# Kernel optimization log

Hardware: AMD Instinct MI355X
Metric: run time of the kernel (lower is better)

## Reference

```python
import jax, jax.numpy as jnp
import numpy as np

# dims
B_, L_, DIN, H, DOUT, NL = 2, 1024, 512, 768, 512, 4
ED, N, K = H, 16, 4            # expand_factor=1 -> d_inner=H; d_state=16; d_conv=4
DTR = (H + 15) // 16           # dt_rank = ceil(d_model/16) = 48


def setup_inputs() -> dict:
    key = jax.random.key(0)
    ks = iter(jax.random.split(key, 32))
    def g(shape, s=0.02):
        return jax.random.normal(next(ks), shape, jnp.float32) * s
    inp = dict(
        x=jax.random.normal(next(ks), (B_, L_, DIN), jnp.float32),
        in_proj_w=g((H, DIN)), in_proj_b=jnp.zeros((H,), jnp.float32),
        out_proj_w=g((DOUT, H)), out_proj_b=jnp.zeros((DOUT,), jnp.float32),
        ln1_w=jnp.ones((NL, H), jnp.float32), ln1_b=jnp.zeros((NL, H), jnp.float32),
        ln2_w=jnp.ones((NL, H), jnp.float32), ln2_b=jnp.zeros((NL, H), jnp.float32),
        ffn_w1=g((NL, 4 * H, H)), ffn_b1=jnp.zeros((NL, 4 * H), jnp.float32),
        ffn_w2=g((NL, H, 4 * H)), ffn_b2=jnp.zeros((NL, H), jnp.float32),
        rms_w=jnp.ones((NL, ED), jnp.float32),
        m_in_w=g((NL, 2 * ED, H)),
        conv_w=g((NL, ED, 1, K), 0.2), conv_b=jnp.zeros((NL, ED), jnp.float32),
        xproj_w=g((NL, DTR + 2 * N, ED)),
        dt_w=g((NL, ED, DTR), 0.1), dt_b=g((NL, ED), 0.1),
        A_log=jnp.log(jnp.tile(jnp.arange(1, N + 1, dtype=jnp.float32), (NL, ED, 1))),
        Dp=jnp.ones((NL, ED), jnp.float32),
        m_out_w=g((NL, H, ED)),
    )
    return inp


def _layernorm(x, w, b):
    m = x.mean(-1, keepdims=True)
    v = ((x - m) ** 2).mean(-1, keepdims=True)
    return (x - m) / jnp.sqrt(v + 1e-5) * w + b


def _rmsnorm(x, w):
    return x * jax.lax.rsqrt((x * x).mean(-1, keepdims=True) + 1e-5) * w


def _selective_scan(dA, dBx):
    # h_t = dA_t * h_{t-1} + dBx_t, done as a parallel associative scan over L
    def comb(c1, c2):
        a1, b1 = c1
        a2, b2 = c2
        return a1 * a2, a2 * b1 + b2
    _, h = jax.lax.associative_scan(comb, (dA, dBx), axis=1)
    return h  # (B, L, ED, N)


def _mamba(x, rw, iw, cw, cb, xw, dw, db, Alog, Dp, ow):
    # mambapy ResidualBlock: x + MambaBlock(RMSNorm(x))
    xn = _rmsnorm(x, rw)
    xz = xn @ iw.T                             # (B, L, 2*ED)
    xi, z = jnp.split(xz, 2, axis=-1)
    # causal depthwise conv1d (padding = K-1 left)
    xc = jax.lax.conv_general_dilated(
        xi.transpose(0, 2, 1), cw, (1,), [(K - 1, 0)],
        feature_group_count=ED, dimension_numbers=('NCH', 'OIH', 'NCH'))
    xi = jax.nn.silu(xc.transpose(0, 2, 1) + cb)
    dbc = xi @ xw.T                            # (B, L, DTR + 2N)
    d = dbc[..., :DTR]
    Bm = dbc[..., DTR:DTR + N]
    Cm = dbc[..., DTR + N:]
    delta = jax.nn.softplus(d @ dw.T + db)     # (B, L, ED)
    A = -jnp.exp(Alog)                         # (ED, N)
    dA = jnp.exp(delta[..., None] * A)         # (B, L, ED, N)
    dBx = (delta * xi)[..., None] * Bm[:, :, None, :]
    h = _selective_scan(dA, dBx)
    y = jnp.einsum('blen,bln->ble', h, Cm) + Dp * xi
    y = y * jax.nn.silu(z)
    return x + y @ ow.T


def reference(x, in_proj_w, in_proj_b, out_proj_w, out_proj_b,
              ln1_w, ln1_b, ln2_w, ln2_b,
              ffn_w1, ffn_b1, ffn_w2, ffn_b2,
              rms_w, m_in_w, conv_w, conv_b, xproj_w,
              dt_w, dt_b, A_log, Dp, m_out_w):
    h = x @ in_proj_w.T + in_proj_b
    for i in range(NL):
        h = h + _mamba(_layernorm(h, ln1_w[i], ln1_b[i]),
                       rms_w[i], m_in_w[i], conv_w[i], conv_b[i], xproj_w[i],
                       dt_w[i], dt_b[i], A_log[i], Dp[i], m_out_w[i])
        hn = _layernorm(h, ln2_w[i], ln2_b[i])
        h = h + jax.nn.relu(hn @ ffn_w1[i].T + ffn_b1[i]) @ ffn_w2[i].T + ffn_b2[i]
    return h @ out_proj_w.T + out_proj_b
```

## Files before the change

kernel.cpp:

```cpp
#include <hip/hip_runtime.h>
#include <stdint.h>

typedef unsigned short u16;
typedef __attribute__((ext_vector_type(8))) short short8;
typedef __attribute__((ext_vector_type(4))) float f32x4;

static __device__ __forceinline__ u16 f2bf(float f){
  unsigned int x = __float_as_uint(f);
  unsigned int r = (x + 0x7FFFu + ((x >> 16) & 1u)) >> 16;
  return (u16)r;
}
static __device__ __forceinline__ float bf2f(u16 u){
  return __uint_as_float(((unsigned int)u) << 16);
}

__global__ __launch_bounds__(256) void prep_cvt(
    const float* __restrict__ s0, const float* __restrict__ s1,
    const float* __restrict__ s2, const float* __restrict__ s3,
    const float* __restrict__ s4, const float* __restrict__ s5,
    const float* __restrict__ s6,
    u16* __restrict__ d0, u16* __restrict__ d1, u16* __restrict__ d2,
    u16* __restrict__ d3, u16* __restrict__ d4, u16* __restrict__ d5,
    u16* __restrict__ d6){
  size_t i = ((size_t)blockIdx.x * 256 + threadIdx.x) * 8;
  const float* src; u16* dst; size_t base;
  if      (i <  1048576){ src = s0; dst = d0; base = 0; }
  else if (i <  1441792){ src = s1; dst = d1; base = 1048576; }
  else if (i <  1835008){ src = s2; dst = d2; base = 1441792; }
  else if (i <  6553600){ src = s3; dst = d3; base = 1835008; }
  else if (i <  8912896){ src = s4; dst = d4; base = 6553600; }
  else if (i < 18350080){ src = s5; dst = d5; base = 8912896; }
  else                  { src = s6; dst = d6; base = 18350080; }
  size_t o = i - base;
  #pragma unroll
  for (int p = 0; p < 2; p++){
    float4 v = *reinterpret_cast<const float4*>(src + o + p * 4);
    union { u16 u[4]; unsigned long long ll; } t;
    t.u[0] = f2bf(v.x); t.u[1] = f2bf(v.y); t.u[2] = f2bf(v.z); t.u[3] = f2bf(v.w);
    *reinterpret_cast<unsigned long long*>(dst + o + p * 4) = t.ll;
  }
}

__global__ __launch_bounds__(256) void build_dbc(const float* __restrict__ dt_w,
                                                 const float* __restrict__ xproj_w,
                                                 u16* __restrict__ out){
  const int total = 4 * 896 * 768;
  for (int idx = blockIdx.x * 256 + threadIdx.x; idx < total; idx += gridDim.x * 256){
    int l = idx / (896 * 768);
    int rem = idx - l * 896 * 768;
    int row = rem / 768;
    int k = rem - row * 768;
    float v = 0.f;
    if (row < 768){
      const float* dtr = dt_w + ((size_t)l * 768 + row) * 48;
      const float* xp  = xproj_w + (size_t)l * 80 * 768 + k;
      #pragma unroll 8
      for (int j = 0; j < 48; j++) v += dtr[j] * xp[(size_t)j * 768];
    } else if (row < 800){
      v = xproj_w[(size_t)l * 80 * 768 + (size_t)(48 + row - 768) * 768 + k];
    }
    out[idx] = f2bf(v);
  }
}

__global__ __launch_bounds__(256) void ln_rms_kernel(const float* __restrict__ in,
                                                     const float* __restrict__ w,
                                                     const float* __restrict__ b,
                                                     const float* __restrict__ rw,
                                                     float* __restrict__ xln,
                                                     u16* __restrict__ outB){
  int row = blockIdx.x;
  const float* x = in + (size_t)row * 768;
  int t = threadIdx.x;
  float v0 = x[t], v1 = x[t + 256], v2 = x[t + 512];
  float s = v0 + v1 + v2;
  float s2 = v0 * v0 + v1 * v1 + v2 * v2;
  #pragma unroll
  for (int off = 1; off < 64; off <<= 1){ s += __shfl_xor(s, off); s2 += __shfl_xor(s2, off); }
  __shared__ float red[8];
  int wid = t >> 6, lane = t & 63;
  if (lane == 0){ red[wid] = s; red[4 + wid] = s2; }
  __syncthreads();
  s = red[0] + red[1] + red[2] + red[3];
  s2 = red[4] + red[5] + red[6] + red[7];
  float mean = s * (1.f / 768.f);
  float var = s2 * (1.f / 768.f) - mean * mean;
  float rstd = rsqrtf(var + 1e-5f);
  float o0 = (v0 - mean) * rstd * w[t] + b[t];
  float o1 = (v1 - mean) * rstd * w[t + 256] + b[t + 256];
  float o2 = (v2 - mean) * rstd * w[t + 512] + b[t + 512];
  xln[(size_t)row * 768 + t]       = o0;
  xln[(size_t)row * 768 + t + 256] = o1;
  xln[(size_t)row * 768 + t + 512] = o2;
  float q = o0 * o0 + o1 * o1 + o2 * o2;
  #pragma unroll
  for (int off = 1; off < 64; off <<= 1){ q += __shfl_xor(q, off); }
  __syncthreads();
  if (lane == 0) red[wid] = q;
  __syncthreads();
  q = red[0] + red[1] + red[2] + red[3];
  float rs = rsqrtf(q * (1.f / 768.f) + 1e-5f);
  outB[(size_t)row * 768 + t]       = f2bf(o0 * rs * rw[t]);
  outB[(size_t)row * 768 + t + 256] = f2bf(o1 * rs * rw[t + 256]);
  outB[(size_t)row * 768 + t + 512] = f2bf(o2 * rs * rw[t + 512]);
}

__global__ __launch_bounds__(256) void ln_kernel(const float* __restrict__ in,
                                                 const float* __restrict__ w,
                                                 const float* __restrict__ b,
                                                 u16* __restrict__ outB){
  int row = blockIdx.x;
  const float* x = in + (size_t)row * 768;
  int t = threadIdx.x;
  float v0 = x[t], v1 = x[t + 256], v2 = x[t + 512];
  float s = v0 + v1 + v2;
  float s2 = v0 * v0 + v1 * v1 + v2 * v2;
  #pragma unroll
  for (int off = 1; off < 64; off <<= 1){ s += __shfl_xor(s, off); s2 += __shfl_xor(s2, off); }
  __shared__ float red[8];
  int wid = t >> 6, lane = t & 63;
  if (lane == 0){ red[wid] = s; red[4 + wid] = s2; }
  __syncthreads();
  s = red[0] + red[1] + red[2] + red[3];
  s2 = red[4] + red[5] + red[6] + red[7];
  float mean = s * (1.f / 768.f);
  float var = s2 * (1.f / 768.f) - mean * mean;
  float rstd = rsqrtf(var + 1e-5f);
  #pragma unroll
  for (int j = 0; j < 3; j++){
    int e = t + j * 256;
    float v = (j == 0) ? v0 : (j == 1) ? v1 : v2;
    outB[(size_t)row * 768 + e] = f2bf((v - mean) * rstd * w[e] + b[e]);
  }
}

__global__ __launch_bounds__(256) void conv_silu(const u16* __restrict__ xzb,
                                                 const float* __restrict__ cw,
                                                 const float* __restrict__ cb,
                                                 u16* __restrict__ xi,
                                                 u16* __restrict__ zs){
  int row = blockIdx.x;
  int b = row >> 10, l = row & 1023;
  for (int e = threadIdx.x; e < 768; e += 256){
    const float* w = cw + (size_t)e * 4;
    float acc = cb[e];
    #pragma unroll
    for (int k = 0; k < 4; k++){
      int ls = l - 3 + k;
      if (ls >= 0) acc += w[k] * bf2f(xzb[((size_t)((b << 10) + ls)) * 1536 + e]);
    }
    float sv = acc / (1.f + __expf(-acc));
    xi[(size_t)row * 768 + e] = f2bf(sv);
    float z = bf2f(xzb[(size_t)row * 1536 + 768 + e]);
    zs[(size_t)row * 768 + e] = f2bf(z / (1.f + __expf(-z)));
  }
}

__global__ __launch_bounds__(256) void scan_pass1(const float* __restrict__ delta,
                                                  const u16* __restrict__ xi,
                                                  const float* __restrict__ bc,
                                                  const float* __restrict__ A_log,
                                                  float2* __restrict__ ab){
  int bid = blockIdx.x;
  int eg = bid % 3; int c = (bid / 3) & 31; int b = bid / 96;
  int e = eg * 256 + threadIdx.x;
  float A[16], a[16], s[16];
  const float* al = A_log + (size_t)e * 16;
  #pragma unroll
  for (int n = 0; n < 16; n++){ A[n] = -__expf(al[n]); a[n] = 1.f; s[n] = 0.f; }
  for (int ll = 0; ll < 32; ll++){
    int row = b * 1024 + c * 32 + ll;
    float dlt = delta[(size_t)row * 768 + e];
    float xiv = bf2f(xi[(size_t)row * 768 + e]);
    float du = dlt * xiv;
    const float* bm = bc + (size_t)row * 32;
    #pragma unroll
    for (int n = 0; n < 16; n++){
      float dA = __expf(dlt * A[n]);
      s[n] = dA * s[n] + du * bm[n];
      a[n] *= dA;
    }
  }
  size_t base = (((size_t)(b * 32 + c) * 768) + e) * 16;
  #pragma unroll
  for (int n = 0; n < 16; n++){ ab[base + n] = make_float2(a[n], s[n]); }
}

__global__ __launch_bounds__(128) void scan_pass2(const float2* __restrict__ ab,
                                                  float* __restrict__ h0){
  int idx = blockIdx.x * 128 + threadIdx.x;
  int b = idx / 12288;
  int en = idx - b * 12288;
  float h = 0.f;
  for (int c = 0; c < 32; c++){
    size_t i = ((size_t)(b * 32 + c) * 12288) + en;
    h0[i] = h;
    float2 v = ab[i];
    h = v.x * h + v.y;
  }
}

__global__ __launch_bounds__(256) void scan_pass3(const float* __restrict__ delta,
                                                  const u16* __restrict__ xi,
                                                  const float* __restrict__ bc,
                                                  const float* __restrict__ A_log,
                                                  const float* __restrict__ h0,
                                                  const float* __restrict__ Dp,
                                                  const u16* __restrict__ zs,
                                                  u16* __restrict__ y){
  int bid = blockIdx.x;
  int eg = bid % 3; int c = (bid / 3) & 31; int b = bid / 96;
  int e = eg * 256 + threadIdx.x;
  float A[16], s[16];
  const float* al = A_log + (size_t)e * 16;
  #pragma unroll
  for (int n = 0; n < 16; n++) A[n] = -__expf(al[n]);
  size_t base = (((size_t)(b * 32 + c) * 768) + e) * 16;
  #pragma unroll
  for (int n = 0; n < 16; n++) s[n] = h0[base + n];
  float dp = Dp[e];
  for (int ll = 0; ll < 32; ll++){
    int row = b * 1024 + c * 32 + ll;
    float dlt = delta[(size_t)row * 768 + e];
    float xiv = bf2f(xi[(size_t)row * 768 + e]);
    float du = dlt * xiv;
    const float* bm = bc + (size_t)row * 32;
    const float* cm = bm + 16;
    float acc = 0.f;
    #pragma unroll
    for (int n = 0; n < 16; n++){
      float dA = __expf(dlt * A[n]);
      s[n] = dA * s[n] + du * bm[n];
      acc += s[n] * cm[n];
    }
    float yv = acc + dp * xiv;
    yv *= bf2f(zs[(size_t)row * 768 + e]);
    y[(size_t)row * 768 + e] = f2bf(yv);
  }
}

template<int MODE, int TS>
__global__ __launch_bounds__(256, 2) void gemmT(
    const u16* __restrict__ A, const u16* __restrict__ Bw, int N, int Kd,
    float* __restrict__ outF, u16* __restrict__ outB,
    const float* __restrict__ bias, const float* __restrict__ r1,
    const float* __restrict__ r2,
    float* __restrict__ dl, float* __restrict__ bco, const float* __restrict__ dtb){
  constexpr int NBUF = (TS == 64) ? 4 : 3;
  constexpr int DEPTH = NBUF - 1;
  constexpr int MI = TS / 32;
  __shared__ u16 sm[NBUF][2 * TS * 64];
  const int tid = threadIdx.x;
  const int wid = tid >> 6, lane = tid & 63;
  const int lhi = lane >> 4, llo = lane & 15;
  const int wm = (wid >> 1) * (TS / 2), wn = (wid & 1) * (TS / 2);
  int nwg = (int)(gridDim.x * gridDim.y);
  int orig = (int)(blockIdx.y * gridDim.x + blockIdx.x);
  int wg = (orig & 7) * (nwg >> 3) + (orig >> 3);
  int gx = (int)gridDim.x;
  int bx = wg % gx, by = wg / gx;
  const int m0 = bx * TS, n0 = by * TS;
  const int nk = Kd >> 6;
  f32x4 acc[MI][MI] = {};

  auto stage = [&](int buf, int kt){
    const u16* Ab = A + (size_t)m0 * Kd + kt * 64;
    const u16* Bb = Bw + (size_t)n0 * Kd + kt * 64;
    u16* basep = &sm[buf][0];
    #pragma unroll
    for (int j = 0; j < TS / 32; j++){
      int sl = j * 256 + tid;
      int row = sl >> 3;
      int ch = (sl & 7) ^ (row & 7);
      __builtin_amdgcn_global_load_lds(
          (const __attribute__((address_space(1))) void*)(Ab + (size_t)row * Kd + ch * 8),
          (__attribute__((address_space(3))) void*)(basep + sl * 8), 16, 0, 0);
    }
    #pragma unroll
    for (int j = 0; j < TS / 32; j++){
      int sl = j * 256 + tid;
      int row = sl >> 3;
      int ch = (sl & 7) ^ (row & 7);
      __builtin_amdgcn_global_load_lds(
          (const __attribute__((address_space(1))) void*)(Bb + (size_t)row * Kd + ch * 8),
          (__attribute__((address_space(3))) void*)(basep + TS * 64 + sl * 8), 16, 0, 0);
    }
  };

  #pragma unroll
  for (int t = 0; t < DEPTH; t++) stage(t, t);
  for (int kt = 0; kt < nk; ++kt){
    if constexpr (TS == 64){
      if (kt + 2 < nk)      asm volatile("s_waitcnt vmcnt(8)" ::: "memory");
      else if (kt + 1 < nk) asm volatile("s_waitcnt vmcnt(4)" ::: "memory");
      else                  asm volatile("s_waitcnt vmcnt(0)" ::: "memory");
    } else {
      if (kt + 1 < nk)      asm volatile("s_waitcnt vmcnt(8)" ::: "memory");
      else                  asm volatile("s_waitcnt vmcnt(0)" ::: "memory");
    }
    __builtin_amdgcn_s_barrier();
    __builtin_amdgcn_sched_barrier(0);
    if (kt + DEPTH < nk) stage((kt + DEPTH) % NBUF, kt + DEPTH);
    const u16* Asb = &sm[kt % NBUF][0];
    const u16* Bsb = &sm[kt % NBUF][TS * 64];
    short8 af[MI][2], bfr[MI][2];
    #pragma unroll
    for (int mi = 0; mi < MI; mi++){
      int row = wm + mi * 16 + llo;
      const u16* rp = Asb + row * 64;
      #pragma unroll
      for (int s2 = 0; s2 < 2; s2++){
        int ch = (s2 * 4 + lhi) ^ (row & 7);
        af[mi][s2] = *(const short8*)(rp + ch * 8);
      }
    }
    #pragma unroll
    for (int ni = 0; ni < MI; ni++){
      int row = wn + ni * 16 + llo;
      const u16* rp = Bsb + row * 64;
      #pragma unroll
      for (int s2 = 0; s2 < 2; s2++){
        int ch = (s2 * 4 + lhi) ^ (row & 7);
        bfr[ni][s2] = *(const short8*)(rp + ch * 8);
      }
    }
    #pragma unroll
    for (int s2 = 0; s2 < 2; s2++)
      #pragma unroll
      for (int mi = 0; mi < MI; mi++)
        #pragma unroll
        for (int ni = 0; ni < MI; ni++)
          acc[mi][ni] = __builtin_amdgcn_mfma_f32_16x16x32_bf16(
              af[mi][s2], bfr[ni][s2], acc[mi][ni], 0, 0, 0);
  }
  #pragma unroll
  for (int mi = 0; mi < MI; mi++){
    #pragma unroll
    for (int ni = 0; ni < MI; ni++){
      int r0 = m0 + wm + mi * 16 + lhi * 4;
      int c = n0 + wn + ni * 16 + llo;
      #pragma unroll
      for (int r = 0; r < 4; r++){
        int rr = r0 + r;
        float v = acc[mi][ni][r];
        if (MODE == 0){
          size_t idx = (size_t)rr * N + c;
          if (bias) v += bias[c];
          if (r1) v += r1[idx];
          if (r2) v += r2[idx];
          outF[idx] = v;
          if (outB) outB[idx] = f2bf(v);
        } else if (MODE == 1){
          size_t idx = (size_t)rr * N + c;
          v += bias[c];
          outB[idx] = f2bf(v > 0.f ? v : 0.f);
        } else if (MODE == 3){
          outB[(size_t)rr * N + c] = f2bf(v);
        } else {
          if (c < 768){
            float tv = v + dtb[c];
            dl[(size_t)rr * 768 + c] = (tv > 20.f) ? tv : log1pf(__expf(tv));
          } else if (c < 800){
            bco[(size_t)rr * 32 + (c - 768)] = v;
          }
        }
      }
    }
  }
}

extern "C" void kernel_launch(void* const* d_in, const int* in_sizes, int n_in,
                              void* d_out, int out_size, void* d_ws, size_t ws_size,
                              hipStream_t stream){
  (void)in_sizes; (void)n_in; (void)out_size; (void)ws_size;
  const float* x_f       = (const float*)d_in[0];
  const float* in_proj_w = (const float*)d_in[1];
  const float* in_proj_b = (const float*)d_in[2];
  const float* out_proj_w= (const float*)d_in[3];
  const float* out_proj_b= (const float*)d_in[4];
  const float* ln1_w     = (const float*)d_in[5];
  const float* ln1_b     = (const float*)d_in[6];
  const float* ln2_w     = (const float*)d_in[7];
  const float* ln2_b     = (const float*)d_in[8];
  const float* ffn_w1    = (const float*)d_in[9];
  const float* ffn_b1    = (const float*)d_in[10];
  const float* ffn_w2    = (const float*)d_in[11];
  const float* ffn_b2    = (const float*)d_in[12];
  const float* rms_w     = (const float*)d_in[13];
  const float* m_in_w    = (const float*)d_in[14];
  const float* conv_w    = (const float*)d_in[15];
  const float* conv_b    = (const float*)d_in[16];
  const float* xproj_w   = (const float*)d_in[17];
  const float* dt_w      = (const float*)d_in[18];
  const float* dt_b      = (const float*)d_in[19];
  const float* A_log     = (const float*)d_in[20];
  const float* Dp        = (const float*)d_in[21];
  const float* m_out_w   = (const float*)d_in[22];

  char* ws = (char*)d_ws;
  size_t off = 0;
  auto alloc = [&](size_t bytes) -> char* {
    char* p = ws + off;
    off += (bytes + 255) & ~(size_t)255;
    return p;
  };
  u16* wb_inp  = (u16*)alloc((size_t)768 * 512 * 2);
  u16* wb_outp = (u16*)alloc((size_t)512 * 768 * 2);
  u16* wb_min  = (u16*)alloc((size_t)4 * 1536 * 768 * 2);
  u16* wb_mout = (u16*)alloc((size_t)4 * 768 * 768 * 2);
  u16* wb_f1   = (u16*)alloc((size_t)4 * 3072 * 768 * 2);
  u16* wb_f2   = (u16*)alloc((size_t)4 * 768 * 3072 * 2);
  u16* wb_dbc  = (u16*)alloc((size_t)4 * 896 * 768 * 2);
  u16* xbf     = (u16*)alloc((size_t)2048 * 512 * 2);
  float* hA    = (float*)alloc((size_t)2048 * 768 * 4);
  float* hB    = (float*)alloc((size_t)2048 * 768 * 4);
  float* xln   = (float*)alloc((size_t)2048 * 768 * 4);
  u16* xnbf    = (u16*)alloc((size_t)2048 * 768 * 2);
  u16* xzb     = (u16*)alloc((size_t)2048 * 1536 * 2);
  u16* xibf    = (u16*)alloc((size_t)2048 * 768 * 2);
  u16* zsbf    = (u16*)alloc((size_t)2048 * 768 * 2);
  float* dltb  = (float*)alloc((size_t)2048 * 768 * 4);
  float* bcb   = (float*)alloc((size_t)2048 * 32 * 4);
  float2* ab   = (float2*)alloc((size_t)2 * 32 * 768 * 16 * 8);
  float* h0    = (float*)alloc((size_t)2 * 32 * 768 * 16 * 4);
  u16* ybf     = (u16*)alloc((size_t)2048 * 768 * 2);
  u16* tbf     = (u16*)alloc((size_t)2048 * 768 * 2);
  u16* f1bf    = (u16*)alloc((size_t)2048 * 3072 * 2);
  u16* hfbf    = (u16*)alloc((size_t)2048 * 768 * 2);

  prep_cvt<<<13568, 256, 0, stream>>>(x_f, in_proj_w, out_proj_w, m_in_w,
                                      m_out_w, ffn_w1, ffn_w2,
                                      xbf, wb_inp, wb_outp, wb_min,
                                      wb_mout, wb_f1, wb_f2);
  build_dbc<<<2048, 256, 0, stream>>>(dt_w, xproj_w, wb_dbc);

  auto gemm64 = [&](int mode, const u16* Ain, const u16* Bww, int N, int K,
                    float* oF, u16* oB, const float* bias, const float* rr1,
                    const float* rr2, float* dl, float* bco, const float* dtb){
    dim3 g(32, N / 64), blk(256);
    if (mode == 0)
      gemmT<0,64><<<g, blk, 0, stream>>>(Ain, Bww, N, K, oF, oB, bias, rr1, rr2, dl, bco, dtb);
    else if (mode == 2)
      gemmT<2,64><<<g, blk, 0, stream>>>(Ain, Bww, N, K, oF, oB, bias, rr1, rr2, dl, bco, dtb);
    else
      gemmT<3,64><<<g, blk, 0, stream>>>(Ain, Bww, N, K, oF, oB, bias, rr1, rr2, dl, bco, dtb);
  };

  gemm64(0, xbf, wb_inp, 768, 512, hA, nullptr, in_proj_b, nullptr, nullptr,
         nullptr, nullptr, nullptr);

  for (int i = 0; i < 4; i++){
    ln_rms_kernel<<<2048, 256, 0, stream>>>(hA, ln1_w + i * 768, ln1_b + i * 768,
                                            rms_w + i * 768, xln, xnbf);
    gemm64(3, xnbf, wb_min + (size_t)i * 1536 * 768, 1536, 768, nullptr, xzb,
           nullptr, nullptr, nullptr, nullptr, nullptr, nullptr);
    conv_silu<<<2048, 256, 0, stream>>>(xzb, conv_w + (size_t)i * 768 * 4,
                                        conv_b + i * 768, xibf, zsbf);
    gemm64(2, xibf, wb_dbc + (size_t)i * 896 * 768, 896, 768, nullptr, nullptr,
           nullptr, nullptr, nullptr, dltb, bcb, dt_b + i * 768);
    scan_pass1<<<192, 256, 0, stream>>>(dltb, xibf, bcb,
                                        A_log + (size_t)i * 768 * 16, ab);
    scan_pass2<<<192, 128, 0, stream>>>(ab, h0);
    scan_pass3<<<192, 256, 0, stream>>>(dltb, xibf, bcb,
                                        A_log + (size_t)i * 768 * 16, h0,
                                        Dp + i * 768, zsbf, ybf);
    gemm64(0, ybf, wb_mout + (size_t)i * 768 * 768, 768, 768, hB, nullptr,
           nullptr, hA, xln, nullptr, nullptr, nullptr);
    ln_kernel<<<2048, 256, 0, stream>>>(hB, ln2_w + i * 768, ln2_b + i * 768, tbf);
    {
      dim3 g(16, 3072 / 128), blk(256);
      gemmT<1,128><<<g, blk, 0, stream>>>(tbf, wb_f1 + (size_t)i * 3072 * 768, 3072, 768,
                                          nullptr, f1bf, ffn_b1 + i * 3072, nullptr,
                                          nullptr, nullptr, nullptr, nullptr);
    }
    gemm64(0, f1bf, wb_f2 + (size_t)i * 768 * 3072, 768, 3072, hA,
           (i == 3) ? hfbf : nullptr, ffn_b2 + i * 768, hB, nullptr,
           nullptr, nullptr, nullptr);
  }
  gemm64(0, hfbf, wb_outp, 512, 768, (float*)d_out, nullptr, out_proj_b,
         nullptr, nullptr, nullptr, nullptr, nullptr);
}
```

Before: 716.6 us.

## Unify GEMMs on 64x64 tiles with XCD-aware mapping and 3-deep buffering

Replaces the TS-templated GEMM with a single 64x64 tile kernel that uses 3 LDS buffers instead of 4, and an occupancy hint of 3 blocks per CU instead of 2. The FFN-up GEMM moves from 128x128 tiles onto the 64x64 kernel. Block-to-tile mapping now assigns 4 consecutive M tiles per XCD so neighbouring blocks share operand rows in L2. MFMA sections are wrapped in s_setprio to favour the compute wave. The costs are a shallower prefetch pipeline and less operand reuse per tile for the large FFN GEMM. The hardcoded mapping assumes gridDim.x is 32, which holds for all current launches.

```diff
diff --git a/kernel.cpp b/kernel.cpp
--- a/kernel.cpp
+++ b/kernel.cpp
@@ -239,36 +239,33 @@
   }
 }
 
-template<int MODE, int TS>
-__global__ __launch_bounds__(256, 2) void gemmT(
+template<int MODE>
+__global__ __launch_bounds__(256, 3) void gemm64(
     const u16* __restrict__ A, const u16* __restrict__ Bw, int N, int Kd,
     float* __restrict__ outF, u16* __restrict__ outB,
     const float* __restrict__ bias, const float* __restrict__ r1,
     const float* __restrict__ r2,
     float* __restrict__ dl, float* __restrict__ bco, const float* __restrict__ dtb){
-  constexpr int NBUF = (TS == 64) ? 4 : 3;
-  constexpr int DEPTH = NBUF - 1;
-  constexpr int MI = TS / 32;
-  __shared__ u16 sm[NBUF][2 * TS * 64];
+  __shared__ u16 sm[3][2 * 64 * 64];
   const int tid = threadIdx.x;
   const int wid = tid >> 6, lane = tid & 63;
   const int lhi = lane >> 4, llo = lane & 15;
-  const int wm = (wid >> 1) * (TS / 2), wn = (wid & 1) * (TS / 2);
-  int nwg = (int)(gridDim.x * gridDim.y);
+  const int wm = (wid >> 1) * 32, wn = (wid & 1) * 32;
   int orig = (int)(blockIdx.y * gridDim.x + blockIdx.x);
-  int wg = (orig & 7) * (nwg >> 3) + (orig >> 3);
-  int gx = (int)gridDim.x;
-  int bx = wg % gx, by = wg / gx;
-  const int m0 = bx * TS, n0 = by * TS;
+  int xcd = orig & 7;
+  int w = orig >> 3;
+  int mt = xcd * 4 + (w & 3);
+  int nt = w >> 2;
+  const int m0 = mt * 64, n0 = nt * 64;
   const int nk = Kd >> 6;
-  f32x4 acc[MI][MI] = {};
+  f32x4 acc[2][2] = {};
 
   auto stage = [&](int buf, int kt){
     const u16* Ab = A + (size_t)m0 * Kd + kt * 64;
     const u16* Bb = Bw + (size_t)n0 * Kd + kt * 64;
     u16* basep = &sm[buf][0];
     #pragma unroll
-    for (int j = 0; j < TS / 32; j++){
+    for (int j = 0; j < 2; j++){
       int sl = j * 256 + tid;
       int row = sl >> 3;
       int ch = (sl & 7) ^ (row & 7);
@@ -277,35 +274,29 @@
           (__attribute__((address_space(3))) void*)(basep + sl * 8), 16, 0, 0);
     }
     #pragma unroll
-    for (int j = 0; j < TS / 32; j++){
+    for (int j = 0; j < 2; j++){
       int sl = j * 256 + tid;
       int row = sl >> 3;
       int ch = (sl & 7) ^ (row & 7);
       __builtin_amdgcn_global_load_lds(
           (const __attribute__((address_space(1))) void*)(Bb + (size_t)row * Kd + ch * 8),
-          (__attribute__((address_space(3))) void*)(basep + TS * 64 + sl * 8), 16, 0, 0);
+          (__attribute__((address_space(3))) void*)(basep + 64 * 64 + sl * 8), 16, 0, 0);
     }
   };
 
-  #pragma unroll
-  for (int t = 0; t < DEPTH; t++) stage(t, t);
+  stage(0, 0);
+  stage(1, 1);
   for (int kt = 0; kt < nk; ++kt){
-    if constexpr (TS == 64){
-      if (kt + 2 < nk)      asm volatile("s_waitcnt vmcnt(8)" ::: "memory");
-      else if (kt + 1 < nk) asm volatile("s_waitcnt vmcnt(4)" ::: "memory");
-      else                  asm volatile("s_waitcnt vmcnt(0)" ::: "memory");
-    } else {
-      if (kt + 1 < nk)      asm volatile("s_waitcnt vmcnt(8)" ::: "memory");
-      else                  asm volatile("s_waitcnt vmcnt(0)" ::: "memory");
-    }
+    if (kt + 1 < nk) asm volatile("s_waitcnt vmcnt(4)" ::: "memory");
+    else             asm volatile("s_waitcnt vmcnt(0)" ::: "memory");
     __builtin_amdgcn_s_barrier();
     __builtin_amdgcn_sched_barrier(0);
-    if (kt + DEPTH < nk) stage((kt + DEPTH) % NBUF, kt + DEPTH);
-    const u16* Asb = &sm[kt % NBUF][0];
-    const u16* Bsb = &sm[kt % NBUF][TS * 64];
-    short8 af[MI][2], bfr[MI][2];
-    #pragma unroll
-    for (int mi = 0; mi < MI; mi++){
+    if (kt + 2 < nk) stage((kt + 2) % 3, kt + 2);
+    const u16* Asb = &sm[kt % 3][0];
+    const u16* Bsb = &sm[kt % 3][64 * 64];
+    short8 af[2][2], bfr[2][2];
+    #pragma unroll
+    for (int mi = 0; mi < 2; mi++){
       int row = wm + mi * 16 + llo;
       const u16* rp = Asb + row * 64;
       #pragma unroll
@@ -315,7 +306,7 @@
       }
     }
     #pragma unroll
-    for (int ni = 0; ni < MI; ni++){
+    for (int ni = 0; ni < 2; ni++){
       int row = wn + ni * 16 + llo;
       const u16* rp = Bsb + row * 64;
       #pragma unroll
@@ -324,19 +315,21 @@
         bfr[ni][s2] = *(const short8*)(rp + ch * 8);
       }
     }
+    __builtin_amdgcn_s_setprio(1);
     #pragma unroll
     for (int s2 = 0; s2 < 2; s2++)
       #pragma unroll
-      for (int mi = 0; mi < MI; mi++)
+      for (int mi = 0; mi < 2; mi++)
         #pragma unroll
-        for (int ni = 0; ni < MI; ni++)
+        for (int ni = 0; ni < 2; ni++)
           acc[mi][ni] = __builtin_amdgcn_mfma_f32_16x16x32_bf16(
               af[mi][s2], bfr[ni][s2], acc[mi][ni], 0, 0, 0);
-  }
-  #pragma unroll
-  for (int mi = 0; mi < MI; mi++){
-    #pragma unroll
-    for (int ni = 0; ni < MI; ni++){
+    __builtin_amdgcn_s_setprio(0);
+  }
+  #pragma unroll
+  for (int mi = 0; mi < 2; mi++){
+    #pragma unroll
+    for (int ni = 0; ni < 2; ni++){
       int r0 = m0 + wm + mi * 16 + lhi * 4;
       int c = n0 + wn + ni * 16 + llo;
       #pragma unroll
@@ -434,49 +427,47 @@
                                       wb_mout, wb_f1, wb_f2);
   build_dbc<<<2048, 256, 0, stream>>>(dt_w, xproj_w, wb_dbc);
 
-  auto gemm64 = [&](int mode, const u16* Ain, const u16* Bww, int N, int K,
-                    float* oF, u16* oB, const float* bias, const float* rr1,
-                    const float* rr2, float* dl, float* bco, const float* dtb){
+  auto gemm = [&](int mode, const u16* Ain, const u16* Bww, int N, int K,
+                  float* oF, u16* oB, const float* bias, const float* rr1,
+                  const float* rr2, float* dl, float* bco, const float* dtb){
     dim3 g(32, N / 64), blk(256);
     if (mode == 0)
-      gemmT<0,64><<<g, blk, 0, stream>>>(Ain, Bww, N, K, oF, oB, bias, rr1, rr2, dl, bco, dtb);
+      gemm64<0><<<g, blk, 0, stream>>>(Ain, Bww, N, K, oF, oB, bias, rr1, rr2, dl, bco, dtb);
+    else if (mode == 1)
+      gemm64<1><<<g, blk, 0, stream>>>(Ain, Bww, N, K, oF, oB, bias, rr1, rr2, dl, bco, dtb);
     else if (mode == 2)
-      gemmT<2,64><<<g, blk, 0, stream>>>(Ain, Bww, N, K, oF, oB, bias, rr1, rr2, dl, bco, dtb);
+      gemm64<2><<<g, blk, 0, stream>>>(Ain, Bww, N, K, oF, oB, bias, rr1, rr2, dl, bco, dtb);
     else
-      gemmT<3,64><<<g, blk, 0, stream>>>(Ain, Bww, N, K, oF, oB, bias, rr1, rr2, dl, bco, dtb);
+      gemm64<3><<<g, blk, 0, stream>>>(Ain, Bww, N, K, oF, oB, bias, rr1, rr2, dl, bco, dtb);
   };
 
-  gemm64(0, xbf, wb_inp, 768, 512, hA, nullptr, in_proj_b, nullptr, nullptr,
-         nullptr, nullptr, nullptr);
+  gemm(0, xbf, wb_inp, 768, 512, hA, nullptr, in_proj_b, nullptr, nullptr,
+       nullptr, nullptr, nullptr);
 
   for (int i = 0; i < 4; i++){
     ln_rms_kernel<<<2048, 256, 0, stream>>>(hA, ln1_w + i * 768, ln1_b + i * 768,
                                             rms_w + i * 768, xln, xnbf);
-    gemm64(3, xnbf, wb_min + (size_t)i * 1536 * 768, 1536, 768, nullptr, xzb,
-           nullptr, nullptr, nullptr, nullptr, nullptr, nullptr);
+    gemm(3, xnbf, wb_min + (size_t)i * 1536 * 768, 1536, 768, nullptr, xzb,
+         nullptr, nullptr, nullptr, nullptr, nullptr, nullptr);
     conv_silu<<<2048, 256, 0, stream>>>(xzb, conv_w + (size_t)i * 768 * 4,
                                         conv_b + i * 768, xibf, zsbf);
-    gemm64(2, xibf, wb_dbc + (size_t)i * 896 * 768, 896, 768, nullptr, nullptr,
-           nullptr, nullptr, nullptr, dltb, bcb, dt_b + i * 768);
+    gemm(2, xibf, wb_dbc + (size_t)i * 896 * 768, 896, 768, nullptr, nullptr,
+         nullptr, nullptr, nullptr, dltb, bcb, dt_b + i * 768);
     scan_pass1<<<192, 256, 0, stream>>>(dltb, xibf, bcb,
                                         A_log + (size_t)i * 768 * 16, ab);
     scan_pass2<<<192, 128, 0, stream>>>(ab, h0);
     scan_pass3<<<192, 256, 0, stream>>>(dltb, xibf, bcb,
                                         A_log + (size_t)i * 768 * 16, h0,
                                         Dp + i * 768, zsbf, ybf);
-    gemm64(0, ybf, wb_mout + (size_t)i * 768 * 768, 768, 768, hB, nullptr,
-           nullptr, hA, xln, nullptr, nullptr, nullptr);
+    gemm(0, ybf, wb_mout + (size_t)i * 768 * 768, 768, 768, hB, nullptr,
+         nullptr, hA, xln, nullptr, nullptr, nullptr);
     ln_kernel<<<2048, 256, 0, stream>>>(hB, ln2_w + i * 768, ln2_b + i * 768, tbf);
-    {
-      dim3 g(16, 3072 / 128), blk(256);
-      gemmT<1,128><<<g, blk, 0, stream>>>(tbf, wb_f1 + (size_t)i * 3072 * 768, 3072, 768,
-                                          nullptr, f1bf, ffn_b1 + i * 3072, nullptr,
-                                          nullptr, nullptr, nullptr, nullptr);
-    }
-    gemm64(0, f1bf, wb_f2 + (size_t)i * 768 * 3072, 768, 3072, hA,
-           (i == 3) ? hfbf : nullptr, ffn_b2 + i * 768, hB, nullptr,
-           nullptr, nullptr, nullptr);
-  }
-  gemm64(0, hfbf, wb_outp, 512, 768, (float*)d_out, nullptr, out_proj_b,
-         nullptr, nullptr, nullptr, nullptr, nullptr);
-}
+    gemm(1, tbf, wb_f1 + (size_t)i * 3072 * 768, 3072, 768, nullptr, f1bf,
+         ffn_b1 + i * 3072, nullptr, nullptr, nullptr, nullptr, nullptr);
+    gemm(0, f1bf, wb_f2 + (size_t)i * 768 * 3072, 768, 3072, hA,
+         (i == 3) ? hfbf : nullptr, ffn_b2 + i * 768, hB, nullptr,
+         nullptr, nullptr, nullptr);
+  }
+  gemm(0, hfbf, wb_outp, 512, 768, (float*)d_out, nullptr, out_proj_b,
+       nullptr, nullptr, nullptr, nullptr, nullptr);
+}
```

After: 680.8 us. 5.0% less time.
